# Optimization experiments

Hardware: AMD Instinct MI355X
Metric: run time of the kernel (lower is better)

Reference implementation:

```python
import jax, jax.numpy as jnp
import numpy as np

M_PER_GROUP = 16
ITER_NUM = 5
EPS = 1e-3


def _iter_norm_whiten(sigma, iter_num=ITER_NUM):
    """Newton-Schulz iteration for Sigma^{-1/2}. sigma: (G, m, m)."""
    g, m, _ = sigma.shape
    eye = jnp.eye(m, dtype=sigma.dtype)
    # normalize by trace so spectral radius < 1
    trace = jnp.trace(sigma, axis1=1, axis2=2)[:, None, None]  # (G,1,1)
    sigma_n = sigma / trace
    P = jnp.broadcast_to(eye, (g, m, m))
    for _ in range(iter_num):
        P3 = P @ P @ P
        P = 1.5 * P - 0.5 * (P3 @ sigma_n)
    # whitening matrix: Sigma^{-1/2} = P / sqrt(trace)
    return P * jax.lax.rsqrt(trace)


def setup_inputs() -> dict:
    key = jax.random.key(0)
    inputs = jax.random.normal(key, (64, 56, 56, 256), dtype=jnp.float32)
    return {"inputs": inputs}


def reference(inputs) -> jnp.ndarray:
    b, w, h, c = inputs.shape
    group = c // M_PER_GROUP
    # center: channels-first flatten, subtract per-channel batch mean
    x = jnp.transpose(inputs, (3, 0, 1, 2)).reshape(c, -1)  # (c, N)
    m = jnp.mean(x, axis=1, keepdims=True)                  # (c, 1)
    f = x - m
    n = f.shape[1]
    fg = f.reshape(group, M_PER_GROUP, n)                   # (G, m, N)
    # per-group covariance
    cov = jnp.einsum('gmn,gkn->gmk', fg, fg) / n            # (G, m, m)
    eye = jnp.eye(M_PER_GROUP, dtype=inputs.dtype)
    sigma = (1.0 - EPS) * cov + EPS * eye
    wm = _iter_norm_whiten(sigma)                           # (G, m, m)
    # whiten
    f_hat = wm @ fg                                         # (G, m, N)
    decorrelated = f_hat.reshape(c, b, w, h)
    return jnp.transpose(decorrelated, (1, 2, 3, 0))        # (b, w, h, c)
```

## Files before the change

### kernel.cpp

```cpp
#include <hip/hip_runtime.h>


constexpr int CCH = 256;
constexpr float EPSV = 1e-3f;
constexpr int PSTRIDE = 4352;
constexpr int STATBLK = 1792;

#define QB(S, comp) __int_as_float(__builtin_amdgcn_update_dpp( \
    0, __float_as_int(comp), (S) * 0x55, 0xF, 0xF, 1))
#define ROT1(comp) __int_as_float(__builtin_amdgcn_update_dpp( \
    0, __float_as_int(comp), 0x39, 0xF, 0xF, 1))
#define ROT2(comp) __int_as_float(__builtin_amdgcn_update_dpp( \
    0, __float_as_int(comp), 0x4E, 0xF, 0xF, 1))

#define FMA4(C, V, U) \
    { C.x += (V).x * (U); C.y += (V).y * (U); C.z += (V).z * (U); C.w += (V).w * (U); }

#define ACCPOS(V)                                                         \
    {                                                                     \
        ss.x += (V).x; ss.y += (V).y; ss.z += (V).z; ss.w += (V).w;       \
        d0 += (V).x * (V).x; d1 += (V).x * (V).y;                         \
        d2 += (V).x * (V).z; d3 += (V).x * (V).w;                         \
        d4 += (V).y * (V).y; d5 += (V).y * (V).z;                         \
        d6 += (V).y * (V).w; d7 += (V).z * (V).z;                         \
        d8 += (V).z * (V).w; d9 += (V).w * (V).w;                         \
        {                                                                 \
            float4 u;                                                     \
            u.x = ROT1((V).x); u.y = ROT1((V).y);                         \
            u.z = ROT1((V).z); u.w = ROT1((V).w);                         \
            FMA4(mA, u, (V).x) FMA4(mB, u, (V).y)                         \
            FMA4(mC, u, (V).z) FMA4(mD, u, (V).w)                         \
        }                                                                 \
        {                                                                 \
            float4 u;                                                     \
            u.x = ROT2((V).x); u.y = ROT2((V).y);                         \
            u.z = ROT2((V).z); u.w = ROT2((V).w);                         \
            FMA4(nA, u, (V).x) FMA4(nB, u, (V).y)                         \
            FMA4(nC, u, (V).z) FMA4(nD, u, (V).w)                         \
        }                                                                 \
    }

constexpr int SLOTF = 4416;

#define SW(RI, CJ, VAL)  sl[gbase + (RI) * 16 + (CJ)] = (VAL);
#define SWM(RI, CJ, VAL) { sl[gbase + (RI) * 16 + (CJ)] = (VAL); \
                           sl[gbase + (CJ) * 16 + (RI)] = (VAL); }
#define SR(RI, CJ, VAR)  VAR += sl[gbase + (RI) * 16 + (CJ)];

#define SLOT_WRITE()                                                        \
    {                                                                       \
        const int R = 4 * rr, A = 4 * c1, B = 4 * c2;                       \
        SW(R+0, R+0, d0) SWM(R+0, R+1, d1) SWM(R+0, R+2, d2)                \
        SWM(R+0, R+3, d3) SW(R+1, R+1, d4) SWM(R+1, R+2, d5)                \
        SWM(R+1, R+3, d6) SW(R+2, R+2, d7) SWM(R+2, R+3, d8)                \
        SW(R+3, R+3, d9)                                                    \
        SWM(R+0, A+0, mA.x) SWM(R+0, A+1, mA.y) SWM(R+0, A+2, mA.z)         \
        SWM(R+0, A+3, mA.w) SWM(R+1, A+0, mB.x) SWM(R+1, A+1, mB.y)         \
        SWM(R+1, A+2, mB.z) SWM(R+1, A+3, mB.w) SWM(R+2, A+0, mC.x)         \
        SWM(R+2, A+1, mC.y) SWM(R+2, A+2, mC.z) SWM(R+2, A+3, mC.w)         \
        SWM(R+3, A+0, mD.x) SWM(R+3, A+1, mD.y) SWM(R+3, A+2, mD.z)         \
        SWM(R+3, A+3, mD.w)                                                 \
        SW(R+0, B+0, nA.x) SW(R+0, B+1, nA.y) SW(R+0, B+2, nA.z)            \
        SW(R+0, B+3, nA.w) SW(R+1, B+0, nB.x) SW(R+1, B+1, nB.y)            \
        SW(R+1, B+2, nB.z) SW(R+1, B+3, nB.w) SW(R+2, B+0, nC.x)            \
        SW(R+2, B+1, nC.y) SW(R+2, B+2, nC.z) SW(R+2, B+3, nC.w)            \
        SW(R+3, B+0, nD.x) SW(R+3, B+1, nD.y) SW(R+3, B+2, nD.z)            \
        SW(R+3, B+3, nD.w)                                                  \
        sl[4160 + lane * 4 + 0] = ss.x; sl[4160 + lane * 4 + 1] = ss.y;     \
        sl[4160 + lane * 4 + 2] = ss.z; sl[4160 + lane * 4 + 3] = ss.w;     \
    }

#define SLOT_ADD()                                                          \
    {                                                                       \
        const int R = 4 * rr, A = 4 * c1, B = 4 * c2;                       \
        SR(R+0, R+0, d0) SR(R+0, R+1, d1) SR(R+0, R+2, d2)                  \
        SR(R+0, R+3, d3) SR(R+1, R+1, d4) SR(R+1, R+2, d5)                  \
        SR(R+1, R+3, d6) SR(R+2, R+2, d7) SR(R+2, R+3, d8)                  \
        SR(R+3, R+3, d9)                                                    \
        SR(R+0, A+0, mA.x) SR(R+0, A+1, mA.y) SR(R+0, A+2, mA.z)            \
        SR(R+0, A+3, mA.w) SR(R+1, A+0, mB.x) SR(R+1, A+1, mB.y)            \
        SR(R+1, A+2, mB.z) SR(R+1, A+3, mB.w) SR(R+2, A+0, mC.x)            \
        SR(R+2, A+1, mC.y) SR(R+2, A+2, mC.z) SR(R+2, A+3, mC.w)            \
        SR(R+3, A+0, mD.x) SR(R+3, A+1, mD.y) SR(R+3, A+2, mD.z)            \
        SR(R+3, A+3, mD.w)                                                  \
        SR(R+0, B+0, nA.x) SR(R+0, B+1, nA.y) SR(R+0, B+2, nA.z)            \
        SR(R+0, B+3, nA.w) SR(R+1, B+0, nB.x) SR(R+1, B+1, nB.y)            \
        SR(R+1, B+2, nB.z) SR(R+1, B+3, nB.w) SR(R+2, B+0, nC.x)            \
        SR(R+2, B+1, nC.y) SR(R+2, B+2, nC.z) SR(R+2, B+3, nC.w)            \
        SR(R+3, B+0, nD.x) SR(R+3, B+1, nD.y) SR(R+3, B+2, nD.z)            \
        SR(R+3, B+3, nD.w)                                                  \
        ss.x += sl[4160 + lane * 4 + 0]; ss.y += sl[4160 + lane * 4 + 1];   \
        ss.z += sl[4160 + lane * 4 + 2]; ss.w += sl[4160 + lane * 4 + 3];   \
    }

__global__ __launch_bounds__(256, 7) void k_stats(const float* __restrict__ x,
                                                  float* __restrict__ partial,
                                                  int npos) {
    const int tid = threadIdx.x;
    const int lane = tid & 63;
    const int w = tid >> 6;
    const int wave = blockIdx.x * 4 + w;
    const int nwaves = gridDim.x * 4;
    const int g = lane >> 2;
    const int rr = lane & 3;
    const int c1 = (rr + 1) & 3;
    const int c2 = (rr + 2) & 3;
    const int gbase = g * 260;

    float4 ss = {0.f, 0.f, 0.f, 0.f};
    float d0 = 0.f, d1 = 0.f, d2 = 0.f, d3 = 0.f, d4 = 0.f, d5 = 0.f,
          d6 = 0.f, d7 = 0.f, d8 = 0.f, d9 = 0.f;
    float4 mA = ss, mB = ss, mC = ss, mD = ss;
    float4 nA = ss, nB = ss, nC = ss, nD = ss;

    const float* bx = x + lane * 4;

    int p = wave;
    if (p < npos) {
        float4 va = *reinterpret_cast<const float4*>(bx + (size_t)p * CCH);
        while (true) {
            const int pn = p + nwaves;
            const bool more = pn < npos;
            float4 vn = va;
            if (more) vn = *reinterpret_cast<const float4*>(bx + (size_t)pn * CCH);
            ACCPOS(va);
            if (!more) break;
            p = pn;
            va = vn;
        }
    }

    __shared__ float sl[SLOTF];

    if (w == 1) SLOT_WRITE();
    __syncthreads();
    if (w == 0) SLOT_ADD();
    __syncthreads();
    if (w == 3) SLOT_WRITE();
    __syncthreads();
    if (w == 2) SLOT_ADD();
    __syncthreads();
    if (w == 2) SLOT_WRITE();
    __syncthreads();
    if (w == 0) { SLOT_ADD(); SLOT_WRITE(); }
    __syncthreads();

    float* rec = partial + (size_t)blockIdx.x * PSTRIDE;
    for (int c = tid; c < 256; c += blockDim.x)
        rec[c] = sl[4160 + c];
    for (int e = tid; e < 4096; e += blockDim.x) {
        const int gg = e >> 8, row = (e >> 4) & 15, col = e & 15;
        rec[256 + e] = sl[gg * 260 + row * 16 + col];
    }
}

__global__ __launch_bounds__(256) void k_reduce(const float* __restrict__ partial,
                                                float* __restrict__ finalv,
                                                int nblk, int nchunks) {
    const int t = blockIdx.x * blockDim.x + threadIdx.x;
    const int total = nchunks * PSTRIDE;
    if (t >= total) return;
    const int chunk = t / PSTRIDE;
    const int e = t - chunk * PSTRIDE;
    const int r0 = chunk * 64;
    const int rend = (r0 + 64 < nblk) ? r0 + 64 : nblk;
    const float* src = partial + (size_t)r0 * PSTRIDE + e;
    float acc = 0.f;
    for (int r = r0; r < rend; ++r, src += PSTRIDE) acc += *src;
    atomicAdd(&finalv[e], acc);
}

__global__ __launch_bounds__(256) void k_wm(const float* __restrict__ sums,
                                            const float* __restrict__ covs,
                                            float* __restrict__ mean,
                                            float* __restrict__ wm,
                                            float inv_n) {
    const int g = blockIdx.x;
    const int tid = threadIdx.x;
    const int i = tid >> 4;
    const int j = tid & 15;

    __shared__ float mu[16];
    __shared__ float sig[16][17];
    __shared__ float P[16][17];
    __shared__ float T[16][17];
    __shared__ float U[16][17];

    if (tid < 16) {
        float m = sums[g * 16 + tid] * inv_n;
        mu[tid] = m;
        mean[g * 16 + tid] = m;
    }
    __syncthreads();

    const float cov = covs[(g * 16 + i) * 16 + j] * inv_n - mu[i] * mu[j];
    const float s = (1.0f - EPSV) * cov + ((i == j) ? EPSV : 0.0f);
    sig[i][j] = s;
    __syncthreads();

    float tr = 0.f;
#pragma unroll
    for (int k = 0; k < 16; ++k) tr += sig[k][k];
    __syncthreads();

    sig[i][j] = s / tr;
    P[i][j] = (i == j) ? 1.0f : 0.0f;
    __syncthreads();

    for (int it = 0; it < 5; ++it) {
        float a = 0.f;
#pragma unroll
        for (int k = 0; k < 16; ++k) a += P[i][k] * P[k][j];
        T[i][j] = a;
        __syncthreads();

        float b = 0.f;
#pragma unroll
        for (int k = 0; k < 16; ++k) b += T[i][k] * P[k][j];
        U[i][j] = b;
        __syncthreads();

        float c = 0.f;
#pragma unroll
        for (int k = 0; k < 16; ++k) c += U[i][k] * sig[k][j];
        const float pn = 1.5f * P[i][j] - 0.5f * c;
        __syncthreads();
        P[i][j] = pn;
        __syncthreads();
    }

    wm[(g * 16 + i) * 16 + j] = P[i][j] * rsqrtf(tr);
}

__global__ __launch_bounds__(256) void k_whiten(const float* __restrict__ x,
                                                const float* __restrict__ mean,
                                                const float* __restrict__ wm,
                                                float* __restrict__ out,
                                                int npos) {
    const int tid = threadIdx.x;
    const int lane = tid & 63;
    const int wave = blockIdx.x * (blockDim.x >> 6) + (tid >> 6);
    const int nwaves = gridDim.x * (blockDim.x >> 6);
    const int g = lane >> 2;
    const int i0 = (lane & 3) * 4;

    float w[4][16];
    const float* wg = wm + g * 256;
#pragma unroll
    for (int a = 0; a < 4; ++a)
#pragma unroll
        for (int j = 0; j < 16; ++j) w[a][j] = wg[(i0 + a) * 16 + j];

    const float4 mu4 = *reinterpret_cast<const float4*>(mean + lane * 4);
    const float* bx = x + lane * 4;
    float* bo = out + lane * 4;

    int p = wave;
    if (p >= npos) return;
    float4 v = *reinterpret_cast<const float4*>(bx + (size_t)p * CCH);
    while (true) {
        const int pn = p + nwaves;
        const bool more = pn < npos;
        float4 vn = v;
        if (more) vn = *reinterpret_cast<const float4*>(bx + (size_t)pn * CCH);

        v.x -= mu4.x; v.y -= mu4.y; v.z -= mu4.z; v.w -= mu4.w;
        float acc[4] = {0.f, 0.f, 0.f, 0.f};
#define WSTEP(S)                                                         \
        {                                                                \
            const float u0 = QB(S, v.x), u1 = QB(S, v.y),                \
                        u2 = QB(S, v.z), u3 = QB(S, v.w);                \
            _Pragma("unroll")                                            \
            for (int a = 0; a < 4; ++a) {                                \
                acc[a] += w[a][(S) * 4 + 0] * u0 + w[a][(S) * 4 + 1] * u1 \
                        + w[a][(S) * 4 + 2] * u2 + w[a][(S) * 4 + 3] * u3; \
            }                                                            \
        }
        WSTEP(0) WSTEP(1) WSTEP(2) WSTEP(3)
#undef WSTEP
        float4 o;
        o.x = acc[0]; o.y = acc[1]; o.z = acc[2]; o.w = acc[3];
        *reinterpret_cast<float4*>(bo + (size_t)p * CCH) = o;

        if (!more) break;
        p = pn;
        v = vn;
    }
}

extern "C" void kernel_launch(void* const* d_in, const int* in_sizes, int n_in,
                              void* d_out, int out_size, void* d_ws, size_t ws_size,
                              hipStream_t stream) {
    const float* x = (const float*)d_in[0];
    float* out = (float*)d_out;
    float* ws = (float*)d_ws;

    const int total = in_sizes[0];
    const int npos = total / CCH;
    const float inv_n = 1.0f / (float)npos;

    float* finalv = ws;
    float* mean = ws + 4352;
    float* wm = ws + 4608;
    float* partial = ws + 8704;

    long avail = (long)(ws_size / 4) - 8704;
    int nblk = (int)(avail / PSTRIDE);
    if (nblk > STATBLK) nblk = STATBLK;
    if (nblk < 64) nblk = 64;

    hipMemsetAsync(d_ws, 0, 4352 * sizeof(float), stream);

    k_stats<<<nblk, 256, 0, stream>>>(x, partial, npos);
    const int nchunks = (nblk + 63) / 64;
    const int rthreads = nchunks * PSTRIDE;
    k_reduce<<<(rthreads + 255) / 256, 256, 0, stream>>>(partial, finalv, nblk, nchunks);
    k_wm<<<16, 256, 0, stream>>>(finalv, finalv + 256, mean, wm, inv_n);
    k_whiten<<<2048, 256, 0, stream>>>(x, mean, wm, out, npos);
}
```

Before: 160.6 us.

## Use two-stage reduction without atomics, nontemporal output stores, more stat blocks

The atomic-add reduction, and the memset it needed, are replaced by two deterministic kernels: per-chunk partial sums are written to a scratch buffer, then summed per element. The whiten kernel's output stores become nontemporal so the large output stream does not pollute cache. The stats kernel's block cap rises to 2048 and its occupancy hint of 7 is dropped. This trades one extra kernel launch for removing the memset and the atomic contention.

```diff
diff --git a/kernel.cpp b/kernel.cpp
--- a/kernel.cpp
+++ b/kernel.cpp
@@ -4,7 +4,9 @@
 constexpr int CCH = 256;
 constexpr float EPSV = 1e-3f;
 constexpr int PSTRIDE = 4352;
-constexpr int STATBLK = 1792;
+constexpr int STATBLK = 2048;
+
+typedef float f32x4 __attribute__((ext_vector_type(4)));
 
 #define QB(S, comp) __int_as_float(__builtin_amdgcn_update_dpp( \
     0, __float_as_int(comp), (S) * 0x55, 0xF, 0xF, 1))
@@ -93,9 +95,9 @@
         ss.z += sl[4160 + lane * 4 + 2]; ss.w += sl[4160 + lane * 4 + 3];   \
     }
 
-__global__ __launch_bounds__(256, 7) void k_stats(const float* __restrict__ x,
-                                                  float* __restrict__ partial,
-                                                  int npos) {
+__global__ __launch_bounds__(256) void k_stats(const float* __restrict__ x,
+                                               float* __restrict__ partial,
+                                               int npos) {
     const int tid = threadIdx.x;
     const int lane = tid & 63;
     const int w = tid >> 6;
@@ -154,9 +156,9 @@
     }
 }
 
-__global__ __launch_bounds__(256) void k_reduce(const float* __restrict__ partial,
-                                                float* __restrict__ finalv,
-                                                int nblk, int nchunks) {
+__global__ __launch_bounds__(256) void k_reduce1(const float* __restrict__ partial,
+                                                 float* __restrict__ p2,
+                                                 int nblk, int nchunks) {
     const int t = blockIdx.x * blockDim.x + threadIdx.x;
     const int total = nchunks * PSTRIDE;
     if (t >= total) return;
@@ -167,7 +169,18 @@
     const float* src = partial + (size_t)r0 * PSTRIDE + e;
     float acc = 0.f;
     for (int r = r0; r < rend; ++r, src += PSTRIDE) acc += *src;
-    atomicAdd(&finalv[e], acc);
+    p2[(size_t)chunk * PSTRIDE + e] = acc;
+}
+
+__global__ __launch_bounds__(256) void k_reduce2(const float* __restrict__ p2,
+                                                 float* __restrict__ finalv,
+                                                 int nchunks) {
+    const int e = blockIdx.x * blockDim.x + threadIdx.x;
+    if (e >= PSTRIDE) return;
+    const float* s = p2 + e;
+    float acc = 0.f;
+    for (int c = 0; c < nchunks; ++c, s += PSTRIDE) acc += *s;
+    finalv[e] = acc;
 }
 
 __global__ __launch_bounds__(256) void k_wm(const float* __restrict__ sums,
@@ -278,9 +291,9 @@
         }
         WSTEP(0) WSTEP(1) WSTEP(2) WSTEP(3)
 #undef WSTEP
-        float4 o;
+        f32x4 o;
         o.x = acc[0]; o.y = acc[1]; o.z = acc[2]; o.w = acc[3];
-        *reinterpret_cast<float4*>(bo + (size_t)p * CCH) = o;
+        __builtin_nontemporal_store(o, reinterpret_cast<f32x4*>(bo + (size_t)p * CCH));
 
         if (!more) break;
         p = pn;
@@ -304,17 +317,18 @@
     float* wm = ws + 4608;
     float* partial = ws + 8704;
 
-    long avail = (long)(ws_size / 4) - 8704;
+    long avail = (long)(ws_size / 4) - 8704 - 32 * PSTRIDE;
     int nblk = (int)(avail / PSTRIDE);
     if (nblk > STATBLK) nblk = STATBLK;
     if (nblk < 64) nblk = 64;
 
-    hipMemsetAsync(d_ws, 0, 4352 * sizeof(float), stream);
+    float* p2 = partial + (size_t)nblk * PSTRIDE;
 
     k_stats<<<nblk, 256, 0, stream>>>(x, partial, npos);
     const int nchunks = (nblk + 63) / 64;
-    const int rthreads = nchunks * PSTRIDE;
-    k_reduce<<<(rthreads + 255) / 256, 256, 0, stream>>>(partial, finalv, nblk, nchunks);
+    const int r1threads = nchunks * PSTRIDE;
+    k_reduce1<<<(r1threads + 255) / 256, 256, 0, stream>>>(partial, p2, nblk, nchunks);
+    k_reduce2<<<(PSTRIDE + 255) / 256, 256, 0, stream>>>(p2, finalv, nchunks);
     k_wm<<<16, 256, 0, stream>>>(finalv, finalv + 256, mean, wm, inv_n);
     k_whiten<<<2048, 256, 0, stream>>>(x, mean, wm, out, npos);
 }
```

New measurement: 150.3 us. 1.07x faster.
